# Optimization experiments

Hardware: AMD Instinct MI355X
Metric: run time of the kernel (lower is better)

Reference implementation:

```python
import jax, jax.numpy as jnp
import numpy as np

HEADS = 8


def setup_inputs() -> dict:
    key = jax.random.key(0)
    ks = jax.random.split(key, 12)
    B, H, W, C = 2, 128, 256, 256
    inner = C  # num_heads * dim_head = 8 * 32

    def p(k, shape):
        return jax.random.normal(k, shape, dtype=jnp.float32) * 0.02

    return {
        "x": jax.random.normal(ks[0], (B, H * W, C), dtype=jnp.float32),
        "Wq_h": p(ks[1], (C, inner)),
        "Wk_h": p(ks[2], (C, inner)),
        "Wv_h": p(ks[3], (C, inner)),
        "Wo_h": p(ks[4], (inner, C)),
        "bo_h": p(ks[5], (C,)),
        "Wq_w": p(ks[6], (C, inner)),
        "Wk_w": p(ks[7], (C, inner)),
        "Wv_w": p(ks[8], (C, inner)),
        "Wo_w": p(ks[9], (inner, C)),
        "bo_w": p(ks[10], (C,)),
        "h": H,
        "w": W,
    }


def reference(x, Wq_h, Wk_h, Wv_h, Wo_h, bo_h, Wq_w, Wk_w, Wv_w, Wo_w, bo_w, h, w):
    b, n, c = x.shape
    heads = HEADS
    d = Wq_h.shape[1] // heads  # dim_head
    scale = d ** -0.5
    xs = x.reshape(b, h, w, c)  # [B,H,W,C]

    def proj(Wm):
        # [B,H,W,heads,d]
        return (xs @ Wm).reshape(b, h, w, heads, d)

    # --- height-axis attention: each column attends across all rows ---
    q, k, v = proj(Wq_h), proj(Wk_h), proj(Wv_h)
    s = jnp.einsum('bxwnd,bywnd->bwnxy', q, k) * scale  # [B,W,heads,H,H]
    a = jax.nn.softmax(s, axis=-1)
    oh = jnp.einsum('bwnxy,bywnd->bxwnd', a, v).reshape(b, h, w, heads * d)
    oh = oh @ Wo_h + bo_h

    # --- width-axis attention: each row attends across all columns ---
    q, k, v = proj(Wq_w), proj(Wk_w), proj(Wv_w)
    s = jnp.einsum('bhxnd,bhynd->bhnxy', q, k) * scale  # [B,H,heads,W,W]
    a = jax.nn.softmax(s, axis=-1)
    ow = jnp.einsum('bhnxy,bhynd->bhxnd', a, v).reshape(b, h, w, heads * d)
    ow = ow @ Wo_w + bo_w

    return (oh + ow).reshape(b, n, c)
```

## Files before the change

kernel.cpp:

```cpp
#include <hip/hip_runtime.h>
#include <hip/hip_bf16.h>
#include <stdint.h>

typedef unsigned short u16;
typedef short bf16x8 __attribute__((ext_vector_type(8)));
typedef float f32x4  __attribute__((ext_vector_type(4)));
typedef float f32x16 __attribute__((ext_vector_type(16)));
typedef unsigned int u32x4 __attribute__((ext_vector_type(4)));

__device__ __forceinline__ u16 f2bf(float f) {
    uint32_t u = __builtin_bit_cast(uint32_t, f);
    u += 0x7fffu + ((u >> 16) & 1u);
    return (u16)(u >> 16);
}

#if __has_builtin(__builtin_amdgcn_exp2f)
#define EXP2(x) __builtin_amdgcn_exp2f(x)
#else
extern "C" __device__ float __ocml_native_exp2_f32(float);
#define EXP2(x) __ocml_native_exp2_f32(x)
#endif

__device__ __forceinline__ void gl_lds16(const u16* g, u16* l) {
    __builtin_amdgcn_global_load_lds(
        (__attribute__((address_space(1))) void*)(g),
        (__attribute__((address_space(3))) void*)(l),
        16, 0, 0);
}

#define MM 65536
#define CC 256

#define QSCALE (1.4426950408889634f * 0.17677669529663687f)

__device__ __forceinline__ int perm_h(int t) {
    return ((t >> 15) << 15) | ((t & 127) << 8) | ((t >> 7) & 255);
}


__global__ void prep_kernel(
    const float* __restrict__ Wq_h, const float* __restrict__ Wk_h, const float* __restrict__ Wv_h,
    const float* __restrict__ Wo_h, const float* __restrict__ bo_h,
    const float* __restrict__ Wq_w, const float* __restrict__ Wk_w, const float* __restrict__ Wv_w,
    const float* __restrict__ Wo_w, const float* __restrict__ bo_w,
    u16* __restrict__ Wh_t, u16* __restrict__ Ww_t,
    u16* __restrict__ Woh_t, u16* __restrict__ Wow_t,
    u16* __restrict__ Wocat, float* __restrict__ bias)
{
    const int tid = blockIdx.x * 256 + threadIdx.x;
    const int nth = gridDim.x * 256;

    for (int i = tid; i < 768 * 256; i += nth) {
        int n = i >> 8, kk = i & 255;
        int which = n >> 8, nn = n & 255;
        const float* Wsh = (which == 0) ? Wq_h : (which == 1) ? Wk_h : Wv_h;
        const float* Wsw = (which == 0) ? Wq_w : (which == 1) ? Wk_w : Wv_w;
        Wh_t[i] = f2bf(Wsh[kk * 256 + nn]);
        Ww_t[i] = f2bf(Wsw[kk * 256 + nn]);
    }
    for (int i = tid; i < 256 * 256; i += nth) {
        int n = i >> 8, k = i & 255;
        Woh_t[i] = f2bf(Wo_h[k * 256 + n]);
        Wow_t[i] = f2bf(Wo_w[k * 256 + n]);
    }
    for (int i = tid; i < 256 * 512; i += nth) {
        int n = i >> 9, k = i & 511;
        float v = (k < 256) ? Wo_h[k * 256 + n] : Wo_w[(k - 256) * 256 + n];
        Wocat[i] = f2bf(v);
    }
    for (int i = tid; i < 256; i += nth) bias[i] = bo_h[i] + bo_w[i];
}

__global__ __launch_bounds__(256) void xcvt_kernel(const float* __restrict__ x, u16* __restrict__ xb)
{
    int i = blockIdx.x * 256 + threadIdx.x;
    const int nth = gridDim.x * 256;
    const int total = MM * 256 / 8;
    for (; i < total; i += nth) {
        const float* ap = x + (size_t)i * 8;
        float4 f0 = *(const float4*)ap;
        float4 f1 = *(const float4*)(ap + 4);
        u16 o[8] = { f2bf(f0.x), f2bf(f0.y), f2bf(f0.z), f2bf(f0.w),
                     f2bf(f1.x), f2bf(f1.y), f2bf(f1.z), f2bf(f1.w) };
        *(int4*)(xb + (size_t)i * 8) = *(const int4*)o;
    }
}

template<int PH, int XB>
__global__ __launch_bounds__(512) void gemm_qk_kernel(
    const float* __restrict__ x, const u16* __restrict__ xb, const u16* __restrict__ Bt,
    u16* __restrict__ Qb, u16* __restrict__ Kb)
{
    constexpr int S = PH ? 128 : 256;
    constexpr int L = PH ? 7 : 8;
    const int K = 256;
    __shared__ u16 sh[24576];
    u16* As = sh;
    u16* Bs = sh + 16384;
    const int tid = threadIdx.x;
    const int lane = tid & 63, wave = tid >> 6;
    const int wm = wave >> 1, wn = wave & 1;
    const int l15 = lane & 15, lq = lane >> 4;

    const int id = blockIdx.x;
    const int xcd = id & 7, wq = id >> 3;
    const int mt = xcd * 32 + (wq >> 2), nt = wq & 3;
    const int m0 = mt * 256, n0 = nt * 128;

    f32x4 acc[4][4];
#pragma unroll
    for (int i = 0; i < 4; i++)
#pragma unroll
        for (int j = 0; j < 4; j++)
#pragma unroll
            for (int t = 0; t < 4; t++) acc[i][j][t] = 0.0f;

    for (int kt = 0; kt < K; kt += 64) {
        __syncthreads();
        if constexpr (XB) {
#pragma unroll
            for (int i = 0; i < 4; i++) {
                int cid = i * 512 + tid;
                int r = cid >> 3, sc = cid & 7;
                int gk = kt + ((sc ^ (r & 7)) << 3);
                int rm = PH ? perm_h(m0 + r) : (m0 + r);
                gl_lds16(xb + (size_t)rm * 256 + gk, As + cid * 8);
            }
#pragma unroll
            for (int i = 0; i < 2; i++) {
                int cid = i * 512 + tid;
                int r = cid >> 3, sc = cid & 7;
                int gk = kt + ((sc ^ (r & 7)) << 3);
                gl_lds16(Bt + (size_t)(n0 + r) * K + gk, Bs + cid * 8);
            }
        } else {
#pragma unroll
            for (int i = 0; i < 4; i++) {
                int cid = i * 512 + tid;
                int r = cid >> 3, sc = cid & 7;
                int gk = kt + ((sc ^ (r & 7)) << 3);
                int rm = PH ? perm_h(m0 + r) : (m0 + r);
                const float* ap = x + (size_t)rm * 256 + gk;
                float4 f0 = *(const float4*)ap;
                float4 f1 = *(const float4*)(ap + 4);
                u16 o[8] = { f2bf(f0.x), f2bf(f0.y), f2bf(f0.z), f2bf(f0.w),
                             f2bf(f1.x), f2bf(f1.y), f2bf(f1.z), f2bf(f1.w) };
                *(int4*)(As + (size_t)cid * 8) = *(const int4*)o;
            }
#pragma unroll
            for (int i = 0; i < 2; i++) {
                int cid = i * 512 + tid;
                int r = cid >> 3, sc = cid & 7;
                int gk = kt + ((sc ^ (r & 7)) << 3);
                *(int4*)(Bs + (size_t)cid * 8) = *(const int4*)(Bt + (size_t)(n0 + r) * K + gk);
            }
        }
        __syncthreads();
#pragma unroll
        for (int ks = 0; ks < 2; ks++) {
            bf16x8 af[4], bfr[4];
#pragma unroll
            for (int i = 0; i < 4; i++) {
                int row = wm * 64 + i * 16 + l15;
                int ca  = ks * 4 + lq;
                af[i]  = *(const bf16x8*)(As + row * 64 + ((ca ^ (row & 7)) << 3));
                int nn  = wn * 64 + i * 16 + l15;
                bfr[i] = *(const bf16x8*)(Bs + nn * 64 + ((ca ^ (nn & 7)) << 3));
            }
#pragma unroll
            for (int i = 0; i < 4; i++)
#pragma unroll
                for (int j = 0; j < 4; j++)
                    acc[i][j] = __builtin_amdgcn_mfma_f32_16x16x32_bf16(af[i], bfr[j], acc[i][j], 0, 0, 0);
        }
    }

    const float scale = (nt < 2) ? (float)QSCALE : 1.0f;
    u16* dstb = (nt < 2) ? Qb : Kb;
    const int ln_ = lane & 31, lh_ = lane >> 5;
    const int hg = wave & 3;
    const int half = wave >> 2;
    const int head = (nt & 1) * 4 + hg;

#pragma unroll
    for (int p = 0; p < 2; p++) {
        __syncthreads();
        if ((wm >> 1) == p) {
#pragma unroll
            for (int i = 0; i < 4; i++)
#pragma unroll
                for (int j = 0; j < 4; j++)
#pragma unroll
                    for (int r = 0; r < 4; r++) {
                        int row = (wm & 1) * 64 + i * 16 + lq * 4 + r;
                        int col = wn * 64 + j * 16 + l15;
                        sh[row * 128 + (col ^ ((row & 7) << 3))] = f2bf(acc[i][j][r] * scale);
                    }
        }
        __syncthreads();
        int base = m0 + p * 128;
        int gi = base >> L;
        int seqbase = base & (S - 1);
        u16* dst = dstb + ((size_t)(gi * 8 + head) * S + seqbase) * 32;
#pragma unroll
        for (int qt = 0; qt < 4; qt++) {
            int row  = qt * 32 + ln_;
            int colb = hg * 32 + half * 16 + lh_ * 8;
            int4 v = *(const int4*)(sh + row * 128 + (colb ^ ((row & 7) << 3)));
            *(int4*)(dst + qt * 1024 + half * 512 + lane * 8) = v;
        }
    }
}

template<int PH, int XB>
__global__ __launch_bounds__(256) void gemm_vt_kernel(
    const u16* __restrict__ Wt, const float* __restrict__ x, const u16* __restrict__ xb,
    u16* __restrict__ Vb)
{
    constexpr int S = PH ? 128 : 256;
    const int K = 256;
    __shared__ u16 sh[XB ? 32768 : 16384];
    const int tid = threadIdx.x;
    const int lane = tid & 63, wave = tid >> 6;
    const int wm = wave & 1, wn = wave >> 1;
    const int l15 = lane & 15, lq = lane >> 4;
    const int m0 = blockIdx.y * 128, n0 = blockIdx.x * 128;

    f32x4 acc[4][4];
#pragma unroll
    for (int i = 0; i < 4; i++)
#pragma unroll
        for (int j = 0; j < 4; j++)
#pragma unroll
            for (int t = 0; t < 4; t++) acc[i][j][t] = 0.0f;

    auto mma_tile = [&](const u16* As, const u16* Bs) {
#pragma unroll
        for (int ks = 0; ks < 2; ks++) {
            bf16x8 af[4], bfr[4];
#pragma unroll
            for (int i = 0; i < 4; i++) {
                int row = wm * 64 + i * 16 + l15;
                int ca  = ks * 4 + lq;
                af[i]  = *(const bf16x8*)(As + row * 64 + ((ca ^ (row & 7)) << 3));
                int nn  = wn * 64 + i * 16 + l15;
                bfr[i] = *(const bf16x8*)(Bs + nn * 64 + ((ca ^ (nn & 7)) << 3));
            }
#pragma unroll
            for (int i = 0; i < 4; i++)
#pragma unroll
                for (int j = 0; j < 4; j++)
                    acc[i][j] = __builtin_amdgcn_mfma_f32_16x16x32_bf16(af[i], bfr[j], acc[i][j], 0, 0, 0);
        }
    };

    if constexpr (XB) {
        u16* As_[2] = { sh,        sh + 16384 };
        u16* Bs_[2] = { sh + 8192, sh + 24576 };
        auto stage = [&](int kt, int buf) {
#pragma unroll
            for (int i = 0; i < 4; i++) {
                int cid = i * 256 + tid;
                int r = cid >> 3, sc = cid & 7;
                int gk = kt + ((sc ^ (r & 7)) << 3);
                gl_lds16(Wt + (size_t)(m0 + r) * K + gk, As_[buf] + cid * 8);
                int cm = PH ? perm_h(n0 + r) : (n0 + r);
                gl_lds16(xb + (size_t)cm * 256 + gk, Bs_[buf] + cid * 8);
            }
        };
        stage(0, 0);
        __syncthreads();
#pragma unroll
        for (int t = 0; t < 4; t++) {
            if (t + 1 < 4) stage((t + 1) * 64, (t + 1) & 1);
            mma_tile(As_[t & 1], Bs_[t & 1]);
            __syncthreads();
        }
    } else {
        u16* As = sh;
        u16* Bs = sh + 8192;
        for (int kt = 0; kt < K; kt += 64) {
            __syncthreads();
#pragma unroll
            for (int i = 0; i < 4; i++) {
                int cid = i * 256 + tid;
                int r = cid >> 3, sc = cid & 7;
                int gk = kt + ((sc ^ (r & 7)) << 3);
                *(int4*)(As + (size_t)cid * 8) = *(const int4*)(Wt + (size_t)(m0 + r) * K + gk);
                int cm = PH ? perm_h(n0 + r) : (n0 + r);
                const float* bp = x + (size_t)cm * 256 + gk;
                float4 f0 = *(const float4*)bp;
                float4 f1 = *(const float4*)(bp + 4);
                u16 o[8] = { f2bf(f0.x), f2bf(f0.y), f2bf(f0.z), f2bf(f0.w),
                             f2bf(f1.x), f2bf(f1.y), f2bf(f1.z), f2bf(f1.w) };
                *(int4*)(Bs + (size_t)cid * 8) = *(const int4*)o;
            }
            __syncthreads();
            mma_tile(As, Bs);
        }
        __syncthreads();
    }

#pragma unroll
    for (int i = 0; i < 4; i++)
#pragma unroll
        for (int j = 0; j < 4; j++)
#pragma unroll
            for (int r = 0; r < 4; r++) {
                int row = wm * 64 + i * 16 + lq * 4 + r;
                int col = wn * 64 + j * 16 + l15;
                sh[row * 128 + (col ^ ((row & 7) << 3))] = f2bf(acc[i][j][r]);
            }
    __syncthreads();

    const int gi = n0 >> (PH ? 7 : 8);
    const int seqbase = n0 & (S - 1);
    const int head = (m0 >> 5) + wave;
    u16* dst = Vb + ((size_t)(gi * 8 + head) * S + seqbase) * 32;
    const int ln_ = lane & 31, lh_ = lane >> 5;
#pragma unroll
    for (int cl = 0; cl < 4; cl++)
#pragma unroll
        for (int half = 0; half < 2; half++) {
            int row  = wave * 32 + ln_;
            int colb = cl * 32 + half * 16 + lh_ * 8;
            int4 v = *(const int4*)(sh + row * 128 + (colb ^ ((row & 7) << 3)));
            *(int4*)(dst + cl * 1024 + half * 512 + lane * 8) = v;
        }
}

__global__ __launch_bounds__(512) void gemm_out_fused_kernel(
    const u16* __restrict__ Ah, const u16* __restrict__ Aw,
    const u16* __restrict__ Bcat, float* __restrict__ Cout, const float* __restrict__ bias)
{
    const int K = 512, N = 256;
    __shared__ u16 sh[24576];
    u16* As = sh;
    u16* Bs = sh + 16384;
    const int tid = threadIdx.x;
    const int lane = tid & 63, wave = tid >> 6;
    const int wm = wave >> 1, wn = wave & 1;
    const int l15 = lane & 15, lq = lane >> 4;

    const int id = blockIdx.x;
    const int xcd = id & 7, wq = id >> 3;
    const int mt = xcd * 32 + (wq >> 1), nt = wq & 1;
    const int m0 = mt * 256, n0 = nt * 128;

    f32x4 acc[4][4];
#pragma unroll
    for (int i = 0; i < 4; i++)
#pragma unroll
        for (int j = 0; j < 4; j++)
#pragma unroll
            for (int t = 0; t < 4; t++) acc[i][j][t] = 0.0f;

    for (int kt = 0; kt < K; kt += 64) {
        __syncthreads();
        const u16* Abase = (kt < 256) ? Ah : Aw;
        int koff = kt & 255;
#pragma unroll
        for (int i = 0; i < 4; i++) {
            int cid = i * 512 + tid;
            int r = cid >> 3, sc = cid & 7;
            int gs = (sc ^ (r & 7)) << 3;
            gl_lds16(Abase + (size_t)(m0 + r) * 256 + koff + gs, As + cid * 8);
        }
#pragma unroll
        for (int i = 0; i < 2; i++) {
            int cid = i * 512 + tid;
            int r = cid >> 3, sc = cid & 7;
            int gs = (sc ^ (r & 7)) << 3;
            gl_lds16(Bcat + (size_t)(n0 + r) * K + kt + gs, Bs + cid * 8);
        }
        __syncthreads();
#pragma unroll
        for (int ks = 0; ks < 2; ks++) {
            bf16x8 af[4], bfr[4];
#pragma unroll
            for (int i = 0; i < 4; i++) {
                int row = wm * 64 + i * 16 + l15;
                int ca  = ks * 4 + lq;
                af[i]  = *(const bf16x8*)(As + row * 64 + ((ca ^ (row & 7)) << 3));
                int nn  = wn * 64 + i * 16 + l15;
                bfr[i] = *(const bf16x8*)(Bs + nn * 64 + ((ca ^ (nn & 7)) << 3));
            }
#pragma unroll
            for (int i = 0; i < 4; i++)
#pragma unroll
                for (int j = 0; j < 4; j++)
                    acc[i][j] = __builtin_amdgcn_mfma_f32_16x16x32_bf16(af[i], bfr[j], acc[i][j], 0, 0, 0);
        }
    }
#pragma unroll
    for (int i = 0; i < 4; i++)
#pragma unroll
        for (int j = 0; j < 4; j++)
#pragma unroll
            for (int r = 0; r < 4; r++) {
                int row = m0 + wm * 64 + i * 16 + lq * 4 + r;
                int col = n0 + wn * 64 + j * 16 + l15;
                Cout[(size_t)row * N + col] = acc[i][j][r] + bias[col];
            }
}

template<int MODE>
__global__ __launch_bounds__(256) void gemm_out_kernel(
    const u16* __restrict__ A16, const u16* __restrict__ Bt,
    float* __restrict__ Cout, const float* __restrict__ bias)
{
    const int K = 256, N = 256;
    __shared__ u16 As[128 * 64];
    __shared__ u16 Bs[128 * 64];
    const int tid = threadIdx.x;
    const int lane = tid & 63, wave = tid >> 6;
    const int wm = wave & 1, wn = wave >> 1;
    const int l15 = lane & 15, lq = lane >> 4;
    const int m0 = blockIdx.y * 128, n0 = blockIdx.x * 128;

    f32x4 acc[4][4];
#pragma unroll
    for (int i = 0; i < 4; i++)
#pragma unroll
        for (int j = 0; j < 4; j++)
#pragma unroll
            for (int t = 0; t < 4; t++) acc[i][j][t] = 0.0f;

    for (int kt = 0; kt < K; kt += 64) {
        __syncthreads();
#pragma unroll
        for (int i = 0; i < 4; i++) {
            int cid = i * 256 + tid;
            int r = cid >> 3, sc = cid & 7;
            int gk = kt + ((sc ^ (r & 7)) << 3);
            *(int4*)(As + (size_t)cid * 8) = *(const int4*)(A16 + (size_t)(m0 + r) * K + gk);
            *(int4*)(Bs + (size_t)cid * 8) = *(const int4*)(Bt + (size_t)(n0 + r) * K + gk);
        }
        __syncthreads();
#pragma unroll
        for (int ks = 0; ks < 2; ks++) {
            bf16x8 af[4], bfr[4];
#pragma unroll
            for (int i = 0; i < 4; i++) {
                int row = wm * 64 + i * 16 + l15;
                int ca  = ks * 4 + lq;
                af[i]  = *(const bf16x8*)(As + row * 64 + ((ca ^ (row & 7)) << 3));
                int nn  = wn * 64 + i * 16 + l15;
                bfr[i] = *(const bf16x8*)(Bs + nn * 64 + ((ca ^ (nn & 7)) << 3));
            }
#pragma unroll
            for (int i = 0; i < 4; i++)
#pragma unroll
                for (int j = 0; j < 4; j++)
                    acc[i][j] = __builtin_amdgcn_mfma_f32_16x16x32_bf16(af[i], bfr[j], acc[i][j], 0, 0, 0);
        }
    }
#pragma unroll
    for (int i = 0; i < 4; i++)
#pragma unroll
        for (int j = 0; j < 4; j++)
#pragma unroll
            for (int r = 0; r < 4; r++) {
                int row = m0 + wm * 64 + i * 16 + lq * 4 + r;
                int col = n0 + wn * 64 + j * 16 + l15;
                size_t idx = (size_t)row * N + col;
                if (MODE == 1) Cout[idx] = acc[i][j][r] + bias[col];
                else           Cout[idx] += acc[i][j][r];
            }
}

template<int S, int PH, int NT>
__global__ __launch_bounds__(NT) void attn_kernel(
    const u16* __restrict__ Qb, const u16* __restrict__ Kb,
    const u16* __restrict__ Vb, u16* __restrict__ att)
{
    constexpr int NC = S / 32;
    const int tid = threadIdx.x;
    const int lane = tid & 63;
    const int wave = tid >> 6;
    const int ln = lane & 31;
    const int lh = lane >> 5;

    const int bid = blockIdx.x;
    const int head = bid & 7;
    const int gi = bid >> 3;
    const int qs = wave * 32;
    const int g = gi * 8 + head;

    const u16* Qg = Qb + (size_t)g * S * 32;
    const u16* Kg = Kb + (size_t)g * S * 32;
    const u16* Vg = Vb + (size_t)g * S * 32;

    const u16* qp = Qg + (qs >> 5) * 1024 + lane * 8;
    bf16x8 bq0 = *(const bf16x8*)qp;
    bf16x8 bq1 = *(const bf16x8*)(qp + 512);

    f32x16 kz;
#pragma unroll
    for (int t = 0; t < 16; t++) kz[t] = 0.0f;
    asm("" : "+v"(kz));

    float rs[4] = {0.0f, 0.0f, 0.0f, 0.0f};
    f32x16 oacc;
#pragma unroll
    for (int t = 0; t < 16; t++) oacc[t] = 0.0f;

    const u16* kp0 = Kg + lane * 8;
    const u16* vp0 = Vg + lane * 8;
    bf16x8 ak0 = *(const bf16x8*)kp0;
    bf16x8 ak1 = *(const bf16x8*)(kp0 + 512);
    bf16x8 bv0 = *(const bf16x8*)vp0;
    bf16x8 bv1 = *(const bf16x8*)(vp0 + 512);

    for (int c = 0; c < NC; c++) {
        f32x16 z = __builtin_amdgcn_mfma_f32_32x32x16_bf16(ak0, bq0, kz, 0, 0, 0);
        z = __builtin_amdgcn_mfma_f32_32x32x16_bf16(ak1, bq1, z, 0, 0, 0);

        int cn = (c + 1 < NC) ? c + 1 : c;
        const u16* kp = kp0 + cn * 1024;
        const u16* vp = vp0 + cn * 1024;
        bf16x8 nk0 = *(const bf16x8*)kp;
        bf16x8 nk1 = *(const bf16x8*)(kp + 512);
        bf16x8 nv0 = *(const bf16x8*)vp;
        bf16x8 nv1 = *(const bf16x8*)(vp + 512);

        asm("" : "+v"(z));
        float p[16];
#pragma unroll
        for (int r = 0; r < 16; r++) { p[r] = EXP2(z[r]); rs[r & 3] += p[r]; }

        unsigned w[8];
#pragma unroll
        for (int t = 0; t < 8; t++) {
            unsigned d;
            asm("v_cvt_pk_bf16_f32 %0, %1, %2" : "=v"(d) : "v"(p[2 * t]), "v"(p[2 * t + 1]));
            w[t] = d;
        }
        auto s0 = __builtin_amdgcn_permlane32_swap(w[0], w[2], false, false);
        auto s1 = __builtin_amdgcn_permlane32_swap(w[1], w[3], false, false);
        auto s2 = __builtin_amdgcn_permlane32_swap(w[4], w[6], false, false);
        auto s3 = __builtin_amdgcn_permlane32_swap(w[5], w[7], false, false);
        u32x4 a0 = { (unsigned)s0[0], (unsigned)s1[0], (unsigned)s0[1], (unsigned)s1[1] };
        u32x4 a1 = { (unsigned)s2[0], (unsigned)s3[0], (unsigned)s2[1], (unsigned)s3[1] };
        bf16x8 pa0 = __builtin_bit_cast(bf16x8, a0);
        bf16x8 pa1 = __builtin_bit_cast(bf16x8, a1);

        oacc = __builtin_amdgcn_mfma_f32_32x32x16_bf16(pa0, bv0, oacc, 0, 0, 0);
        oacc = __builtin_amdgcn_mfma_f32_32x32x16_bf16(pa1, bv1, oacc, 0, 0, 0);

        ak0 = nk0; ak1 = nk1; bv0 = nv0; bv1 = nv1;
    }

    float rsum = (rs[0] + rs[1]) + (rs[2] + rs[3]);
    rsum += __shfl_xor(rsum, 32);
    float inv = 1.0f / rsum;
#pragma unroll
    for (int r = 0; r < 16; r++) {
        int row = (r & 3) + ((r >> 2) << 3) + (lh << 2);
        float is = __shfl(inv, row);
        int seq = qs + row;
        int m = PH ? ((gi >> 8) * 32768 + seq * 256 + (gi & 255))
                   : (gi * 256 + seq);
        att[(size_t)m * 256 + head * 32 + ln] = f2bf(oacc[r] * is);
    }
}

extern "C" void kernel_launch(void* const* d_in, const int* in_sizes, int n_in,
                              void* d_out, int out_size, void* d_ws, size_t ws_size,
                              hipStream_t stream)
{
    (void)in_sizes; (void)n_in; (void)out_size;
    const float* x    = (const float*)d_in[0];
    const float* Wq_h = (const float*)d_in[1];
    const float* Wk_h = (const float*)d_in[2];
    const float* Wv_h = (const float*)d_in[3];
    const float* Wo_h = (const float*)d_in[4];
    const float* bo_h = (const float*)d_in[5];
    const float* Wq_w = (const float*)d_in[6];
    const float* Wk_w = (const float*)d_in[7];
    const float* Wv_w = (const float*)d_in[8];
    const float* Wo_w = (const float*)d_in[9];
    const float* bo_w = (const float*)d_in[10];

    const size_t NB = (size_t)MM * 256;
    u16* Qb   = (u16*)d_ws;
    u16* Kb   = Qb + NB;
    u16* Vb   = Kb + NB;
    u16* attb = Vb + NB;
    u16* xb   = attb + NB;
    const size_t WT = (size_t)2 * 768 * 256 + (size_t)2 * 256 * 256 + (size_t)256 * 512 + 512;
    const bool use_xb = ws_size >= (5 * NB + WT) * sizeof(u16);
    u16* wp = use_xb ? (xb + NB) : xb;
    u16* Wh_t  = wp;
    u16* Ww_t  = Wh_t + 768 * 256;
    u16* Woh_t = Ww_t + 768 * 256;
    u16* Wow_t = Woh_t + 256 * 256;
    u16* Wocat = Wow_t + 256 * 256;
    float* bias = (float*)(Wocat + 256 * 512);

    prep_kernel<<<512, 256, 0, stream>>>(Wq_h, Wk_h, Wv_h, Wo_h, bo_h,
                                         Wq_w, Wk_w, Wv_w, Wo_w, bo_w,
                                         Wh_t, Ww_t, Woh_t, Wow_t, Wocat, bias);
    if (use_xb)
        xcvt_kernel<<<8192, 256, 0, stream>>>(x, xb);

    if (use_xb) {
        gemm_qk_kernel<1, 1><<<1024, 512, 0, stream>>>(x, xb, Wh_t, Qb, Kb);
        gemm_vt_kernel<1, 1><<<dim3(512, 2), 256, 0, stream>>>(Wh_t + 512 * 256, x, xb, Vb);
        attn_kernel<128, 1, 256><<<4096, 256, 0, stream>>>(Qb, Kb, Vb, attb);

        gemm_qk_kernel<0, 1><<<1024, 512, 0, stream>>>(x, xb, Ww_t, Qb, Kb);
        gemm_vt_kernel<0, 1><<<dim3(512, 2), 256, 0, stream>>>(Ww_t + 512 * 256, x, xb, Vb);
        attn_kernel<256, 0, 512><<<2048, 512, 0, stream>>>(Qb, Kb, Vb, xb);

        gemm_out_fused_kernel<<<512, 512, 0, stream>>>(attb, xb, Wocat,
                                                       (float*)d_out, bias);
    } else {
        gemm_qk_kernel<1, 0><<<1024, 512, 0, stream>>>(x, xb, Wh_t, Qb, Kb);
        gemm_vt_kernel<1, 0><<<dim3(512, 2), 256, 0, stream>>>(Wh_t + 512 * 256, x, xb, Vb);
        attn_kernel<128, 1, 256><<<4096, 256, 0, stream>>>(Qb, Kb, Vb, attb);
        gemm_out_kernel<1><<<dim3(2, 512), 256, 0, stream>>>(attb, Woh_t, (float*)d_out, bias);

        gemm_qk_kernel<0, 0><<<1024, 512, 0, stream>>>(x, xb, Ww_t, Qb, Kb);
        gemm_vt_kernel<0, 0><<<dim3(512, 2), 256, 0, stream>>>(Ww_t + 512 * 256, x, xb, Vb);
        attn_kernel<256, 0, 512><<<2048, 512, 0, stream>>>(Qb, Kb, Vb, attb);
        gemm_out_kernel<2><<<dim3(2, 512), 256, 0, stream>>>(attb, Wow_t, (float*)d_out, nullptr);
    }
}
```

Baseline: 334.8 us.

## Fuse Q/K and V projection GEMMs into a single QKV kernel

On the bf16-staged path, the separate Q/K GEMM and V^T GEMM launches are merged into one kernel with six N-tiles per M-tile. The two extra tiles compute V and write it transposed via LDS with strided gathers. This cuts one launch per axis and lets the x tile be read by blocks sharing an XCD, but loses the double-buffered V pipeline and adds an uncoalesced-style LDS transpose for V. The fallback path is kept but split into XB-free templates.

```diff
diff --git a/kernel.cpp b/kernel.cpp
--- a/kernel.cpp
+++ b/kernel.cpp
@@ -86,10 +86,10 @@
     }
 }
 
-template<int PH, int XB>
-__global__ __launch_bounds__(512) void gemm_qk_kernel(
-    const float* __restrict__ x, const u16* __restrict__ xb, const u16* __restrict__ Bt,
-    u16* __restrict__ Qb, u16* __restrict__ Kb)
+template<int PH>
+__global__ __launch_bounds__(512) void gemm_qkv_kernel(
+    const u16* __restrict__ xb, const u16* __restrict__ Bt,
+    u16* __restrict__ Qb, u16* __restrict__ Kb, u16* __restrict__ Vb)
 {
     constexpr int S = PH ? 128 : 256;
     constexpr int L = PH ? 7 : 8;
@@ -104,7 +104,7 @@
 
     const int id = blockIdx.x;
     const int xcd = id & 7, wq = id >> 3;
-    const int mt = xcd * 32 + (wq >> 2), nt = wq & 3;
+    const int mt = xcd * 32 + wq / 6, nt = wq % 6;
     const int m0 = mt * 256, n0 = nt * 128;
 
     f32x4 acc[4][4];
@@ -117,43 +117,20 @@
 
     for (int kt = 0; kt < K; kt += 64) {
         __syncthreads();
-        if constexpr (XB) {
-#pragma unroll
-            for (int i = 0; i < 4; i++) {
-                int cid = i * 512 + tid;
-                int r = cid >> 3, sc = cid & 7;
-                int gk = kt + ((sc ^ (r & 7)) << 3);
-                int rm = PH ? perm_h(m0 + r) : (m0 + r);
-                gl_lds16(xb + (size_t)rm * 256 + gk, As + cid * 8);
-            }
-#pragma unroll
-            for (int i = 0; i < 2; i++) {
-                int cid = i * 512 + tid;
-                int r = cid >> 3, sc = cid & 7;
-                int gk = kt + ((sc ^ (r & 7)) << 3);
-                gl_lds16(Bt + (size_t)(n0 + r) * K + gk, Bs + cid * 8);
-            }
-        } else {
-#pragma unroll
-            for (int i = 0; i < 4; i++) {
-                int cid = i * 512 + tid;
-                int r = cid >> 3, sc = cid & 7;
-                int gk = kt + ((sc ^ (r & 7)) << 3);
-                int rm = PH ? perm_h(m0 + r) : (m0 + r);
-                const float* ap = x + (size_t)rm * 256 + gk;
-                float4 f0 = *(const float4*)ap;
-                float4 f1 = *(const float4*)(ap + 4);
-                u16 o[8] = { f2bf(f0.x), f2bf(f0.y), f2bf(f0.z), f2bf(f0.w),
-                             f2bf(f1.x), f2bf(f1.y), f2bf(f1.z), f2bf(f1.w) };
-                *(int4*)(As + (size_t)cid * 8) = *(const int4*)o;
-            }
-#pragma unroll
-            for (int i = 0; i < 2; i++) {
-                int cid = i * 512 + tid;
-                int r = cid >> 3, sc = cid & 7;
-                int gk = kt + ((sc ^ (r & 7)) << 3);
-                *(int4*)(Bs + (size_t)cid * 8) = *(const int4*)(Bt + (size_t)(n0 + r) * K + gk);
-            }
+#pragma unroll
+        for (int i = 0; i < 4; i++) {
+            int cid = i * 512 + tid;
+            int r = cid >> 3, sc = cid & 7;
+            int gk = kt + ((sc ^ (r & 7)) << 3);
+            int rm = PH ? perm_h(m0 + r) : (m0 + r);
+            gl_lds16(xb + (size_t)rm * 256 + gk, As + cid * 8);
+        }
+#pragma unroll
+        for (int i = 0; i < 2; i++) {
+            int cid = i * 512 + tid;
+            int r = cid >> 3, sc = cid & 7;
+            int gk = kt + ((sc ^ (r & 7)) << 3);
+            gl_lds16(Bt + (size_t)(n0 + r) * K + gk, Bs + cid * 8);
         }
         __syncthreads();
 #pragma unroll
@@ -175,6 +152,158 @@
         }
     }
 
+    const int ln_ = lane & 31, lh_ = lane >> 5;
+
+    if (nt < 4) {
+        const float scale = (nt < 2) ? (float)QSCALE : 1.0f;
+        u16* dstb = (nt < 2) ? Qb : Kb;
+        const int hg = wave & 3;
+        const int half = wave >> 2;
+        const int head = (nt & 1) * 4 + hg;
+
+#pragma unroll
+        for (int p = 0; p < 2; p++) {
+            __syncthreads();
+            if ((wm >> 1) == p) {
+#pragma unroll
+                for (int i = 0; i < 4; i++)
+#pragma unroll
+                    for (int j = 0; j < 4; j++)
+#pragma unroll
+                        for (int r = 0; r < 4; r++) {
+                            int row = (wm & 1) * 64 + i * 16 + lq * 4 + r;
+                            int col = wn * 64 + j * 16 + l15;
+                            sh[row * 128 + (col ^ ((row & 7) << 3))] = f2bf(acc[i][j][r] * scale);
+                        }
+            }
+            __syncthreads();
+            int base = m0 + p * 128;
+            int gi = base >> L;
+            int seqbase = base & (S - 1);
+            u16* dst = dstb + ((size_t)(gi * 8 + head) * S + seqbase) * 32;
+#pragma unroll
+            for (int qt = 0; qt < 4; qt++) {
+                int row  = qt * 32 + ln_;
+                int colb = hg * 32 + half * 16 + lh_ * 8;
+                int4 v = *(const int4*)(sh + row * 128 + (colb ^ ((row & 7) << 3)));
+                *(int4*)(dst + qt * 1024 + half * 512 + lane * 8) = v;
+            }
+        }
+    } else {
+        const int hh = wave & 3;
+        const int tq = wave >> 2;
+        const int head = (nt - 4) * 4 + hh;
+
+#pragma unroll
+        for (int p = 0; p < 2; p++) {
+            __syncthreads();
+            if ((wm >> 1) == p) {
+#pragma unroll
+                for (int i = 0; i < 4; i++)
+#pragma unroll
+                    for (int j = 0; j < 4; j++)
+#pragma unroll
+                        for (int r = 0; r < 4; r++) {
+                            int row = (wm & 1) * 64 + i * 16 + lq * 4 + r;
+                            int col = wn * 64 + j * 16 + l15;
+                            sh[row * 128 + (col ^ ((row & 7) << 3))] = f2bf(acc[i][j][r]);
+                        }
+            }
+            __syncthreads();
+            int base = m0 + p * 128;
+            int gi = base >> L;
+            int seqbase = base & (S - 1);
+            u16* dst = Vb + ((size_t)(gi * 8 + head) * S + seqbase) * 32;
+#pragma unroll
+            for (int tt = 0; tt < 2; tt++) {
+                int t = tq * 2 + tt;
+#pragma unroll
+                for (int half = 0; half < 2; half++) {
+                    u16 o[8];
+#pragma unroll
+                    for (int j = 0; j < 8; j++) {
+                        int row = t * 32 + half * 16 + lh_ * 8 + j;
+                        int col = hh * 32 + ln_;
+                        o[j] = sh[row * 128 + (col ^ ((row & 7) << 3))];
+                    }
+                    *(int4*)(dst + t * 1024 + half * 512 + lane * 8) = *(const int4*)o;
+                }
+            }
+        }
+    }
+}
+
+template<int PH>
+__global__ __launch_bounds__(512) void gemm_qk_kernel(
+    const float* __restrict__ x, const u16* __restrict__ Bt,
+    u16* __restrict__ Qb, u16* __restrict__ Kb)
+{
+    constexpr int S = PH ? 128 : 256;
+    constexpr int L = PH ? 7 : 8;
+    const int K = 256;
+    __shared__ u16 sh[24576];
+    u16* As = sh;
+    u16* Bs = sh + 16384;
+    const int tid = threadIdx.x;
+    const int lane = tid & 63, wave = tid >> 6;
+    const int wm = wave >> 1, wn = wave & 1;
+    const int l15 = lane & 15, lq = lane >> 4;
+
+    const int id = blockIdx.x;
+    const int xcd = id & 7, wq = id >> 3;
+    const int mt = xcd * 32 + (wq >> 2), nt = wq & 3;
+    const int m0 = mt * 256, n0 = nt * 128;
+
+    f32x4 acc[4][4];
+#pragma unroll
+    for (int i = 0; i < 4; i++)
+#pragma unroll
+        for (int j = 0; j < 4; j++)
+#pragma unroll
+            for (int t = 0; t < 4; t++) acc[i][j][t] = 0.0f;
+
+    for (int kt = 0; kt < K; kt += 64) {
+        __syncthreads();
+#pragma unroll
+        for (int i = 0; i < 4; i++) {
+            int cid = i * 512 + tid;
+            int r = cid >> 3, sc = cid & 7;
+            int gk = kt + ((sc ^ (r & 7)) << 3);
+            int rm = PH ? perm_h(m0 + r) : (m0 + r);
+            const float* ap = x + (size_t)rm * 256 + gk;
+            float4 f0 = *(const float4*)ap;
+            float4 f1 = *(const float4*)(ap + 4);
+            u16 o[8] = { f2bf(f0.x), f2bf(f0.y), f2bf(f0.z), f2bf(f0.w),
+                         f2bf(f1.x), f2bf(f1.y), f2bf(f1.z), f2bf(f1.w) };
+            *(int4*)(As + (size_t)cid * 8) = *(const int4*)o;
+        }
+#pragma unroll
+        for (int i = 0; i < 2; i++) {
+            int cid = i * 512 + tid;
+            int r = cid >> 3, sc = cid & 7;
+            int gk = kt + ((sc ^ (r & 7)) << 3);
+            *(int4*)(Bs + (size_t)cid * 8) = *(const int4*)(Bt + (size_t)(n0 + r) * K + gk);
+        }
+        __syncthreads();
+#pragma unroll
+        for (int ks = 0; ks < 2; ks++) {
+            bf16x8 af[4], bfr[4];
+#pragma unroll
+            for (int i = 0; i < 4; i++) {
+                int row = wm * 64 + i * 16 + l15;
+                int ca  = ks * 4 + lq;
+                af[i]  = *(const bf16x8*)(As + row * 64 + ((ca ^ (row & 7)) << 3));
+                int nn  = wn * 64 + i * 16 + l15;
+                bfr[i] = *(const bf16x8*)(Bs + nn * 64 + ((ca ^ (nn & 7)) << 3));
+            }
+#pragma unroll
+            for (int i = 0; i < 4; i++)
+#pragma unroll
+                for (int j = 0; j < 4; j++)
+                    acc[i][j] = __builtin_amdgcn_mfma_f32_16x16x32_bf16(af[i], bfr[j], acc[i][j], 0, 0, 0);
+        }
+    }
+
     const float scale = (nt < 2) ? (float)QSCALE : 1.0f;
     u16* dstb = (nt < 2) ? Qb : Kb;
     const int ln_ = lane & 31, lh_ = lane >> 5;
@@ -212,14 +341,15 @@
     }
 }
 
-template<int PH, int XB>
+template<int PH>
 __global__ __launch_bounds__(256) void gemm_vt_kernel(
-    const u16* __restrict__ Wt, const float* __restrict__ x, const u16* __restrict__ xb,
-    u16* __restrict__ Vb)
+    const u16* __restrict__ Wt, const float* __restrict__ x, u16* __restrict__ Vb)
 {
     constexpr int S = PH ? 128 : 256;
     const int K = 256;
-    __shared__ u16 sh[XB ? 32768 : 16384];
+    __shared__ u16 sh[16384];
+    u16* As = sh;
+    u16* Bs = sh + 8192;
     const int tid = threadIdx.x;
     const int lane = tid & 63, wave = tid >> 6;
     const int wm = wave & 1, wn = wave >> 1;
@@ -234,7 +364,23 @@
 #pragma unroll
             for (int t = 0; t < 4; t++) acc[i][j][t] = 0.0f;
 
-    auto mma_tile = [&](const u16* As, const u16* Bs) {
+    for (int kt = 0; kt < K; kt += 64) {
+        __syncthreads();
+#pragma unroll
+        for (int i = 0; i < 4; i++) {
+            int cid = i * 256 + tid;
+            int r = cid >> 3, sc = cid & 7;
+            int gk = kt + ((sc ^ (r & 7)) << 3);
+            *(int4*)(As + (size_t)cid * 8) = *(const int4*)(Wt + (size_t)(m0 + r) * K + gk);
+            int cm = PH ? perm_h(n0 + r) : (n0 + r);
+            const float* bp = x + (size_t)cm * 256 + gk;
+            float4 f0 = *(const float4*)bp;
+            float4 f1 = *(const float4*)(bp + 4);
+            u16 o[8] = { f2bf(f0.x), f2bf(f0.y), f2bf(f0.z), f2bf(f0.w),
+                         f2bf(f1.x), f2bf(f1.y), f2bf(f1.z), f2bf(f1.w) };
+            *(int4*)(Bs + (size_t)cid * 8) = *(const int4*)o;
+        }
+        __syncthreads();
 #pragma unroll
         for (int ks = 0; ks < 2; ks++) {
             bf16x8 af[4], bfr[4];
@@ -252,55 +398,9 @@
                 for (int j = 0; j < 4; j++)
                     acc[i][j] = __builtin_amdgcn_mfma_f32_16x16x32_bf16(af[i], bfr[j], acc[i][j], 0, 0, 0);
         }
-    };
-
-    if constexpr (XB) {
-        u16* As_[2] = { sh,        sh + 16384 };
-        u16* Bs_[2] = { sh + 8192, sh + 24576 };
-        auto stage = [&](int kt, int buf) {
-#pragma unroll
-            for (int i = 0; i < 4; i++) {
-                int cid = i * 256 + tid;
-                int r = cid >> 3, sc = cid & 7;
-                int gk = kt + ((sc ^ (r & 7)) << 3);
-                gl_lds16(Wt + (size_t)(m0 + r) * K + gk, As_[buf] + cid * 8);
-                int cm = PH ? perm_h(n0 + r) : (n0 + r);
-                gl_lds16(xb + (size_t)cm * 256 + gk, Bs_[buf] + cid * 8);
-            }
-        };
-        stage(0, 0);
-        __syncthreads();
-#pragma unroll
-        for (int t = 0; t < 4; t++) {
-            if (t + 1 < 4) stage((t + 1) * 64, (t + 1) & 1);
-            mma_tile(As_[t & 1], Bs_[t & 1]);
-            __syncthreads();
-        }
-    } else {
-        u16* As = sh;
-        u16* Bs = sh + 8192;
-        for (int kt = 0; kt < K; kt += 64) {
-            __syncthreads();
-#pragma unroll
-            for (int i = 0; i < 4; i++) {
-                int cid = i * 256 + tid;
-                int r = cid >> 3, sc = cid & 7;
-                int gk = kt + ((sc ^ (r & 7)) << 3);
-                *(int4*)(As + (size_t)cid * 8) = *(const int4*)(Wt + (size_t)(m0 + r) * K + gk);
-                int cm = PH ? perm_h(n0 + r) : (n0 + r);
-                const float* bp = x + (size_t)cm * 256 + gk;
-                float4 f0 = *(const float4*)bp;
-                float4 f1 = *(const float4*)(bp + 4);
-                u16 o[8] = { f2bf(f0.x), f2bf(f0.y), f2bf(f0.z), f2bf(f0.w),
-                             f2bf(f1.x), f2bf(f1.y), f2bf(f1.z), f2bf(f1.w) };
-                *(int4*)(Bs + (size_t)cid * 8) = *(const int4*)o;
-            }
-            __syncthreads();
-            mma_tile(As, Bs);
-        }
-        __syncthreads();
-    }
-
+    }
+
+    __syncthreads();
 #pragma unroll
     for (int i = 0; i < 4; i++)
 #pragma unroll
@@ -605,24 +705,22 @@
         xcvt_kernel<<<8192, 256, 0, stream>>>(x, xb);
 
     if (use_xb) {
-        gemm_qk_kernel<1, 1><<<1024, 512, 0, stream>>>(x, xb, Wh_t, Qb, Kb);
-        gemm_vt_kernel<1, 1><<<dim3(512, 2), 256, 0, stream>>>(Wh_t + 512 * 256, x, xb, Vb);
+        gemm_qkv_kernel<1><<<1536, 512, 0, stream>>>(xb, Wh_t, Qb, Kb, Vb);
         attn_kernel<128, 1, 256><<<4096, 256, 0, stream>>>(Qb, Kb, Vb, attb);
 
-        gemm_qk_kernel<0, 1><<<1024, 512, 0, stream>>>(x, xb, Ww_t, Qb, Kb);
-        gemm_vt_kernel<0, 1><<<dim3(512, 2), 256, 0, stream>>>(Ww_t + 512 * 256, x, xb, Vb);
+        gemm_qkv_kernel<0><<<1536, 512, 0, stream>>>(xb, Ww_t, Qb, Kb, Vb);
         attn_kernel<256, 0, 512><<<2048, 512, 0, stream>>>(Qb, Kb, Vb, xb);
 
         gemm_out_fused_kernel<<<512, 512, 0, stream>>>(attb, xb, Wocat,
                                                        (float*)d_out, bias);
     } else {
-        gemm_qk_kernel<1, 0><<<1024, 512, 0, stream>>>(x, xb, Wh_t, Qb, Kb);
-        gemm_vt_kernel<1, 0><<<dim3(512, 2), 256, 0, stream>>>(Wh_t + 512 * 256, x, xb, Vb);
+        gemm_qk_kernel<1><<<1024, 512, 0, stream>>>(x, Wh_t, Qb, Kb);
+        gemm_vt_kernel<1><<<dim3(512, 2), 256, 0, stream>>>(Wh_t + 512 * 256, x, Vb);
         attn_kernel<128, 1, 256><<<4096, 256, 0, stream>>>(Qb, Kb, Vb, attb);
         gemm_out_kernel<1><<<dim3(2, 512), 256, 0, stream>>>(attb, Woh_t, (float*)d_out, bias);
 
-        gemm_qk_kernel<0, 0><<<1024, 512, 0, stream>>>(x, xb, Ww_t, Qb, Kb);
-        gemm_vt_kernel<0, 0><<<dim3(512, 2), 256, 0, stream>>>(Ww_t + 512 * 256, x, xb, Vb);
+        gemm_qk_kernel<0><<<1024, 512, 0, stream>>>(x, Ww_t, Qb, Kb);
+        gemm_vt_kernel<0><<<dim3(512, 2), 256, 0, stream>>>(Ww_t + 512 * 256, x, Vb);
         attn_kernel<256, 0, 512><<<2048, 512, 0, stream>>>(Qb, Kb, Vb, attb);
         gemm_out_kernel<2><<<dim3(2, 512), 256, 0, stream>>>(attb, Wow_t, (float*)d_out, nullptr);
     }
```

New measurement: 337.9 us. No clear change (+0.9%).
